# Kernel tuning notes

Hardware: AMD Instinct MI355X
Metric: run time of the kernel (lower is better)

The kernel has to match this reference:

```python
import jax, jax.numpy as jnp
import numpy as np


def setup_inputs() -> dict:
    key = jax.random.key(0)
    k1, k2, k3, k4 = jax.random.split(key, 4)
    B, S, E, H = 8, 2048, 1024, 64
    x = jax.random.normal(k1, (B, S, E), dtype=jnp.float32)
    scale = 1.0 / np.sqrt(E)
    Wq = jax.random.normal(k2, (E, H), dtype=jnp.float32) * scale
    Wk = jax.random.normal(k3, (E, H), dtype=jnp.float32) * scale
    Wv = jax.random.normal(k4, (E, H), dtype=jnp.float32) * scale
    return {"x": x, "Wq": Wq, "Wk": Wk, "Wv": Wv}


def reference(x, Wq, Wk, Wv):
    # x: [B, S, E]; Wq/Wk/Wv: [E, H]
    B, S, E = x.shape
    H = Wq.shape[1]
    q = x @ Wq  # [B, S, H]
    k = x @ Wk
    v = x @ Wv
    inv_sqrt_h = 1.0 / jnp.sqrt(jnp.asarray(H, dtype=x.dtype))
    att = jnp.einsum("bqh,bkh->bqk", q, k) * inv_sqrt_h  # [B, S, S]
    causal = jnp.tril(jnp.ones((S, S), dtype=bool))
    att = jnp.where(causal, att, jnp.asarray(-jnp.inf, dtype=att.dtype))
    att = jax.nn.softmax(att, axis=-1)
    # dropout p=0.0 (eval) -> identity
    return jnp.einsum("bqk,bkh->bqh", att, v)  # [B, S, H]
```

## Files before the change

kernel.cpp:

```cpp
#include <hip/hip_runtime.h>
#include <math.h>

typedef __attribute__((ext_vector_type(8))) short bf16x8;
typedef __attribute__((ext_vector_type(16))) float fx16;

#define SEQ 2048
#define HD 64

__device__ __forceinline__ unsigned f2bf_bits(float f){
  unsigned u = __float_as_uint(f);
  return (u + 0x7fffu + ((u >> 16) & 1u)) >> 16;
}
__device__ __forceinline__ unsigned cvt_pk_bf16(float a, float b){
  unsigned r;
  asm("v_cvt_pk_bf16_f32 %0, %1, %2" : "=v"(r) : "v"(a), "v"(b));
  return r;
}
__device__ __forceinline__ float lo16f(unsigned u){ return __uint_as_float(u << 16); }
__device__ __forceinline__ float hi16f(unsigned u){ return __uint_as_float(u & 0xffff0000u); }
union U8 { bf16x8 v; short s[8]; unsigned u[4]; };

__device__ __forceinline__ fx16 mfma_bf16(bf16x8 a, bf16x8 b, fx16 c){
  return __builtin_amdgcn_mfma_f32_32x32x16_bf16(a, b, c, 0, 0, 0);
}
__device__ __forceinline__ fx16 fzero(){
  fx16 z;
#pragma unroll
  for (int i = 0; i < 16; ++i) z[i] = 0.f;
  return z;
}

__global__ __launch_bounds__(256) void wconv_kernel(
    const float* __restrict__ Wq, const float* __restrict__ Wk, const float* __restrict__ Wv,
    short* __restrict__ wsB)
{
  int gid = blockIdx.x * 4 + (threadIdx.x >> 6);
  int lane = threadIdx.x & 63;
  int l31 = lane & 31, h = lane >> 5;
  int half = gid & 1;
  int rem = gid >> 1;
  int t = rem % 6;
  int stage = rem / 6;
  int n = t * 32 + l31;
  int mat = n >> 6, col = n & 63;
  const float* W = (mat == 0) ? Wq : (mat == 1) ? Wk : Wv;
  int kbase = stage * 16 + h * 8;
  U8 o;
#pragma unroll
  for (int i = 0; i < 8; ++i) {
    float f = W[(size_t)(kbase + i) * 64 + col];
    unsigned hb = f2bf_bits(f);
    if (half == 0) o.s[i] = (short)hb;
    else {
      float hf = __uint_as_float(hb << 16);
      o.s[i] = (short)f2bf_bits(f - hf);
    }
  }
  *(bf16x8*)(wsB + (size_t)gid * 512 + lane * 8) = o.v;
}

__global__ __launch_bounds__(256) void proj_kernel(
    const float* __restrict__ x, const short* __restrict__ wsB,
    short* __restrict__ qh, short* __restrict__ ql,
    short* __restrict__ kh, short* __restrict__ kl,
    short* __restrict__ vth, short* __restrict__ vtl)
{
  __shared__ float Rx[6 * 16 * 64];
  __shared__ float Vb[32 * 68];

  const int tid = threadIdx.x;
  const int lane = tid & 63, w = tid >> 6;
  const int l31 = lane & 31, h = lane >> 5;
  const int nsel = w & 1;
  const int ksel = w >> 1;
  const int row0 = blockIdx.x * 32;
  const size_t xbase = (size_t)(row0 + l31) * 1024;

  fx16 acc[3];
#pragma unroll
  for (int t = 0; t < 3; ++t) acc[t] = fzero();

#pragma unroll 4
  for (int s = 0; s < 32; ++s) {
    const int stage = ksel * 32 + s;
    const int k = stage * 16 + h * 8;
    float4 fa = *(const float4*)(x + xbase + k);
    float4 fb = *(const float4*)(x + xbase + k + 4);
    U8 ah, al;
    ah.u[0] = cvt_pk_bf16(fa.x, fa.y);
    ah.u[1] = cvt_pk_bf16(fa.z, fa.w);
    ah.u[2] = cvt_pk_bf16(fb.x, fb.y);
    ah.u[3] = cvt_pk_bf16(fb.z, fb.w);
    al.u[0] = cvt_pk_bf16(fa.x - lo16f(ah.u[0]), fa.y - hi16f(ah.u[0]));
    al.u[1] = cvt_pk_bf16(fa.z - lo16f(ah.u[1]), fa.w - hi16f(ah.u[1]));
    al.u[2] = cvt_pk_bf16(fb.x - lo16f(ah.u[2]), fb.y - hi16f(ah.u[2]));
    al.u[3] = cvt_pk_bf16(fb.z - lo16f(ah.u[3]), fb.w - hi16f(ah.u[3]));
#pragma unroll
    for (int tt = 0; tt < 3; ++tt) {
      const int tg = nsel * 3 + tt;
      const size_t g2 = ((size_t)stage * 6 + tg) * 2;
      bf16x8 Bh = *(const bf16x8*)(wsB + g2 * 512 + lane * 8);
      bf16x8 Bl = *(const bf16x8*)(wsB + g2 * 512 + 512 + lane * 8);
      acc[tt] = mfma_bf16(al.v, Bh, acc[tt]);
      acc[tt] = mfma_bf16(ah.v, Bl, acc[tt]);
      acc[tt] = mfma_bf16(ah.v, Bh, acc[tt]);
    }
  }

  if (ksel == 1) {
#pragma unroll
    for (int t = 0; t < 3; ++t) {
      const int tg = nsel * 3 + t;
#pragma unroll
      for (int r = 0; r < 16; ++r)
        Rx[tg * 1024 + r * 64 + lane] = acc[t][r];
    }
  }
  __syncthreads();
  if (ksel == 0) {
#pragma unroll
    for (int t = 0; t < 3; ++t) {
      const int tg = nsel * 3 + t;
      const int mat = tg >> 1;
      const int colb = (tg & 1) * 32 + l31;
      if (mat < 2) {
        short* dh = (mat == 0) ? qh : kh;
        short* dl = (mat == 0) ? ql : kl;
#pragma unroll
        for (int r = 0; r < 16; ++r) {
          float f = acc[t][r] + Rx[tg * 1024 + r * 64 + lane];
          int rowg = row0 + (r & 3) + 8 * (r >> 2) + 4 * h;
          unsigned hb = f2bf_bits(f);
          float hf = __uint_as_float(hb << 16);
          unsigned lb = f2bf_bits(f - hf);
          dh[(size_t)rowg * 64 + colb] = (short)hb;
          dl[(size_t)rowg * 64 + colb] = (short)lb;
        }
      } else {
#pragma unroll
        for (int r = 0; r < 16; ++r) {
          float f = acc[t][r] + Rx[tg * 1024 + r * 64 + lane];
          int srel = (r & 3) + 8 * (r >> 2) + 4 * h;
          Vb[srel * 68 + (tg - 4) * 32 + l31] = f;
        }
      }
    }
  }
  __syncthreads();
  {
    int d = tid >> 2, s8 = (tid & 3) * 8;
    int bb = row0 >> 11, s0 = row0 & 2047;
    U8 hv, lv;
#pragma unroll
    for (int ss = 0; ss < 8; ++ss) {
      float f = Vb[(s8 + ss) * 68 + d];
      unsigned hb = f2bf_bits(f);
      float hf = __uint_as_float(hb << 16);
      hv.s[ss] = (short)hb;
      lv.s[ss] = (short)f2bf_bits(f - hf);
    }
    size_t o = (size_t)(bb * 64 + d) * 2048 + s0 + s8;
    *(bf16x8*)(vth + o) = hv.v;
    *(bf16x8*)(vtl + o) = lv.v;
  }
}

__global__ __launch_bounds__(64) void attn_kernel(
    const short* __restrict__ qh, const short* __restrict__ ql,
    const short* __restrict__ kh, const short* __restrict__ kl,
    const short* __restrict__ vth, const short* __restrict__ vtl,
    float* __restrict__ segO, float* __restrict__ segL, float* __restrict__ segM)
{
  const int bid = blockIdx.x;
  const int b = bid & 7;
  const int r = bid >> 3;
  int g = 0;
  while (r >= 4 * (g + 1) * (g + 2)) ++g;
  const int rr = r - 4 * g * (g + 1);
  const int qt = g * 8 + rr / (g + 1);
  const int sg = rr % (g + 1);
  const int nk = qt + 1;
  const int nsg = g + 1;
  const int bs = nk / nsg, rem = nk % nsg;
  const int nsteps = bs + (sg < rem ? 1 : 0);
  const int kt0 = sg * bs + (sg < rem ? sg : rem);

  const int lane = threadIdx.x;
  const int l31 = lane & 31, h = lane >> 5;
  const int qabs = qt * 32 + l31;

  bf16x8 qf0[4], qf1[4];
  {
    size_t qrow = ((size_t)b * 2048 + qabs) * 64;
#pragma unroll
    for (int ds = 0; ds < 4; ++ds) {
      qf0[ds] = *(const bf16x8*)(qh + qrow + ds * 16 + 8 * h);
      qf1[ds] = *(const bf16x8*)(ql + qrow + ds * 16 + 8 * h);
    }
  }

  fx16 acc0 = fzero(), acc1 = fzero();
  float Mrun = -3e38f, lrun = 0.f;

  bf16x8 kah[4], kal[4];
  {
    const size_t koff = ((size_t)b * 2048 + (size_t)kt0 * 32 + l31) * 64 + 8 * h;
#pragma unroll
    for (int ds = 0; ds < 4; ++ds) {
      kah[ds] = *(const bf16x8*)(kh + koff + ds * 16);
      kal[ds] = *(const bf16x8*)(kl + koff + ds * 16);
    }
  }

  for (int it = 0; it < nsteps; ++it) {
    const int kt = kt0 + it;
    bf16x8 vfh[2][2], vfl[2][2];
#pragma unroll
    for (int kp = 0; kp < 2; ++kp)
#pragma unroll
      for (int md = 0; md < 2; ++md) {
        const size_t vrow = (size_t)(b * 64 + md * 32 + l31) * 2048 + kt * 32 + kp * 16 + 8 * h;
        vfh[kp][md] = *(const bf16x8*)(vth + vrow);
        vfl[kp][md] = *(const bf16x8*)(vtl + vrow);
      }
    const int kn = (it + 1 < nsteps) ? kt + 1 : kt;
    bf16x8 knh[4], knl[4];
    {
      const size_t koff = ((size_t)b * 2048 + (size_t)kn * 32 + l31) * 64 + 8 * h;
#pragma unroll
      for (int ds = 0; ds < 4; ++ds) {
        knh[ds] = *(const bf16x8*)(kh + koff + ds * 16);
        knl[ds] = *(const bf16x8*)(kl + koff + ds * 16);
      }
    }

    fx16 stA = fzero(), stB = fzero();
    __builtin_amdgcn_s_setprio(1);
#pragma unroll
    for (int ds = 0; ds < 4; ++ds) {
      stA = mfma_bf16(kah[ds], qf0[ds], stA);
      stB = mfma_bf16(kal[ds], qf0[ds], stB);
      stB = mfma_bf16(kah[ds], qf1[ds], stB);
    }
    __builtin_amdgcn_s_setprio(0);

    float sv[16];
    const bool diag = (kt == qt);
#pragma unroll
    for (int r2 = 0; r2 < 16; ++r2) {
      float s = (stA[r2] + stB[r2]) * 0.125f;
      if (diag) {
        int ka = kt * 32 + (r2 & 3) + 8 * (r2 >> 2) + 4 * h;
        if (ka > qabs) s = -3e38f;
      }
      sv[r2] = s;
    }
    float tm = sv[0];
#pragma unroll
    for (int r2 = 1; r2 < 16; ++r2) tm = fmaxf(tm, sv[r2]);
    tm = fmaxf(tm, __shfl_xor(tm, 32, 64));
    float Mnew = fmaxf(Mrun, tm);
    float alpha = __expf(Mrun - Mnew);
    Mrun = Mnew;
    float psum = 0.f;
#pragma unroll
    for (int r2 = 0; r2 < 16; ++r2) { sv[r2] = __expf(sv[r2] - Mnew); psum += sv[r2]; }
    psum += __shfl_xor(psum, 32, 64);
    lrun = lrun * alpha + psum;
#pragma unroll
    for (int r2 = 0; r2 < 16; ++r2) { acc0[r2] *= alpha; acc1[r2] *= alpha; }

    unsigned chv[8], clv[8];
#pragma unroll
    for (int q2 = 0; q2 < 8; ++q2) {
      unsigned c = cvt_pk_bf16(sv[2 * q2], sv[2 * q2 + 1]);
      chv[q2] = c;
      clv[q2] = cvt_pk_bf16(sv[2 * q2] - lo16f(c), sv[2 * q2 + 1] - hi16f(c));
    }
#pragma unroll
    for (int kp = 0; kp < 2; ++kp) {
      U8 ph, pl;
      {
        unsigned c0 = chv[4 * kp], c1 = chv[4 * kp + 1], c2 = chv[4 * kp + 2], c3 = chv[4 * kp + 3];
        unsigned x0 = (unsigned)__shfl_xor((int)c0, 32, 64);
        unsigned x1 = (unsigned)__shfl_xor((int)c1, 32, 64);
        unsigned x2 = (unsigned)__shfl_xor((int)c2, 32, 64);
        unsigned x3 = (unsigned)__shfl_xor((int)c3, 32, 64);
        ph.u[0] = h ? x2 : c0;  ph.u[1] = h ? x3 : c1;
        ph.u[2] = h ? c2 : x0;  ph.u[3] = h ? c3 : x1;
        c0 = clv[4 * kp]; c1 = clv[4 * kp + 1]; c2 = clv[4 * kp + 2]; c3 = clv[4 * kp + 3];
        x0 = (unsigned)__shfl_xor((int)c0, 32, 64);
        x1 = (unsigned)__shfl_xor((int)c1, 32, 64);
        x2 = (unsigned)__shfl_xor((int)c2, 32, 64);
        x3 = (unsigned)__shfl_xor((int)c3, 32, 64);
        pl.u[0] = h ? x2 : c0;  pl.u[1] = h ? x3 : c1;
        pl.u[2] = h ? c2 : x0;  pl.u[3] = h ? c3 : x1;
      }
      __builtin_amdgcn_s_setprio(1);
      acc0 = mfma_bf16(vfl[kp][0], ph.v, acc0);
      acc0 = mfma_bf16(vfh[kp][0], pl.v, acc0);
      acc0 = mfma_bf16(vfh[kp][0], ph.v, acc0);
      acc1 = mfma_bf16(vfl[kp][1], ph.v, acc1);
      acc1 = mfma_bf16(vfh[kp][1], pl.v, acc1);
      acc1 = mfma_bf16(vfh[kp][1], ph.v, acc1);
      __builtin_amdgcn_s_setprio(0);
    }
#pragma unroll
    for (int ds = 0; ds < 4; ++ds) { kah[ds] = knh[ds]; kal[ds] = knl[ds]; }
  }

  float* o = segO + (size_t)bid * 2048;
#pragma unroll
  for (int md = 0; md < 2; ++md) {
#pragma unroll
    for (int r2 = 0; r2 < 16; ++r2) {
      int d = md * 32 + (r2 & 3) + 8 * (r2 >> 2) + 4 * h;
      float val = md ? acc1[r2] : acc0[r2];
      o[d * 32 + l31] = val;
    }
  }
  if (h == 0) {
    segL[(size_t)bid * 32 + l31] = lrun;
    segM[(size_t)bid * 32 + l31] = Mrun;
  }
}

__global__ __launch_bounds__(256) void combine_kernel(
    const float* __restrict__ segO, const float* __restrict__ segL,
    const float* __restrict__ segM, float* __restrict__ out)
{
  __shared__ float Sc[8][32];
  __shared__ float Linv[32];
  __shared__ float Ot[64 * 40];

  const int bq = blockIdx.x;
  const int b = bq >> 6, qt = bq & 63;
  const int g = qt >> 3, nsg = g + 1;
  const int base = 4 * g * (g + 1) + (qt & 7) * nsg;
  const int tid = threadIdx.x;

  if (tid < 32) {
    float M = -3e38f;
    for (int s = 0; s < nsg; ++s)
      M = fmaxf(M, segM[(size_t)((base + s) * 8 + b) * 32 + tid]);
    float L = 0.f;
    for (int s = 0; s < nsg; ++s) {
      float e = __expf(segM[(size_t)((base + s) * 8 + b) * 32 + tid] - M);
      Sc[s][tid] = e;
      L += e * segL[(size_t)((base + s) * 8 + b) * 32 + tid];
    }
    Linv[tid] = 1.f / L;
  }
  __syncthreads();
  {
#pragma unroll
    for (int i = tid; i < 512; i += 256) {
      int d = i >> 3, q4 = (i & 7) * 4;
      float4 acc = {0.f, 0.f, 0.f, 0.f};
      for (int s = 0; s < nsg; ++s) {
        float4 v = *(const float4*)(segO + (size_t)((base + s) * 8 + b) * 2048 + d * 32 + q4);
        acc.x += Sc[s][q4 + 0] * v.x;
        acc.y += Sc[s][q4 + 1] * v.y;
        acc.z += Sc[s][q4 + 2] * v.z;
        acc.w += Sc[s][q4 + 3] * v.w;
      }
      *(float4*)&Ot[d * 40 + q4] = acc;
    }
  }
  __syncthreads();
  {
    const int q = tid >> 3, dc = (tid & 7) * 8;
    const float inv = Linv[q];
    float* dst = out + ((size_t)b * 2048 + qt * 32 + q) * 64 + dc;
#pragma unroll
    for (int i = 0; i < 2; ++i) {
      float4 o;
      o.x = Ot[(dc + 4 * i + 0) * 40 + q] * inv;
      o.y = Ot[(dc + 4 * i + 1) * 40 + q] * inv;
      o.z = Ot[(dc + 4 * i + 2) * 40 + q] * inv;
      o.w = Ot[(dc + 4 * i + 3) * 40 + q] * inv;
      *(float4*)(dst + 4 * i) = o;
    }
  }
}

extern "C" void kernel_launch(void* const* d_in, const int* in_sizes, int n_in,
                              void* d_out, int out_size, void* d_ws, size_t ws_size,
                              hipStream_t stream) {
  const float* x  = (const float*)d_in[0];
  const float* Wq = (const float*)d_in[1];
  const float* Wk = (const float*)d_in[2];
  const float* Wv = (const float*)d_in[3];

  char* wsb = (char*)d_ws;
  short* wsB = (short*)(wsb + 0);
  short* qh  = (short*)(wsb + 786432);
  short* ql  = (short*)(wsb + 2883584);
  short* kh  = (short*)(wsb + 4980736);
  short* kl  = (short*)(wsb + 7077888);
  short* vth = (short*)(wsb + 9175040);
  short* vtl = (short*)(wsb + 11272192);
  float* segO = (float*)(wsb + 13369344);
  float* segL = (float*)(wsb + 32243712);
  float* segM = (float*)(wsb + 32538624);

  wconv_kernel<<<192, 256, 0, stream>>>(Wq, Wk, Wv, wsB);
  proj_kernel<<<512, 256, 0, stream>>>(x, wsB, qh, ql, kh, kl, vth, vtl);
  attn_kernel<<<2304, 64, 0, stream>>>(qh, ql, kh, kl, vth, vtl, segO, segL, segM);
  combine_kernel<<<512, 256, 0, stream>>>(segO, segL, segM, (float*)d_out);
}
```

Measured before the change: 97.79 us.

## Stage projection operands in LDS and split attention into fixed five-tile segments

The projection kernel now runs six waves per block, one per output column tile, with the full K dimension in each wave. Weights go into LDS through async global_load_lds and x is converted to bf16 hi/lo in double-buffered LDS, which removes the split-K reduction through shared memory and the redundant global weight reads. The attention split changes to fixed segments of at most five key tiles, so there are more blocks (3536) with even work, and the K register prefetch is removed. The combine kernel adapts to the new segment indexing. In exchange there are more partial-segment writes and combine reads, and a barrier on every K chunk in the projection.

```diff
diff --git a/kernel.cpp b/kernel.cpp
--- a/kernel.cpp
+++ b/kernel.cpp
@@ -59,95 +59,106 @@
   *(bf16x8*)(wsB + (size_t)gid * 512 + lane * 8) = o.v;
 }
 
-__global__ __launch_bounds__(256) void proj_kernel(
+__global__ __launch_bounds__(384) void proj_kernel(
     const float* __restrict__ x, const short* __restrict__ wsB,
     short* __restrict__ qh, short* __restrict__ ql,
     short* __restrict__ kh, short* __restrict__ kl,
     short* __restrict__ vth, short* __restrict__ vtl)
 {
-  __shared__ float Rx[6 * 16 * 64];
+  __shared__ short Bs[2][12288];
+  __shared__ short Xs[2][2048];
   __shared__ float Vb[32 * 68];
 
   const int tid = threadIdx.x;
   const int lane = tid & 63, w = tid >> 6;
   const int l31 = lane & 31, h = lane >> 5;
-  const int nsel = w & 1;
-  const int ksel = w >> 1;
   const int row0 = blockIdx.x * 32;
-  const size_t xbase = (size_t)(row0 + l31) * 1024;
-
-  fx16 acc[3];
-#pragma unroll
-  for (int t = 0; t < 3; ++t) acc[t] = fzero();
-
-#pragma unroll 4
-  for (int s = 0; s < 32; ++s) {
-    const int stage = ksel * 32 + s;
-    const int k = stage * 16 + h * 8;
-    float4 fa = *(const float4*)(x + xbase + k);
-    float4 fb = *(const float4*)(x + xbase + k + 4);
-    U8 ah, al;
-    ah.u[0] = cvt_pk_bf16(fa.x, fa.y);
-    ah.u[1] = cvt_pk_bf16(fa.z, fa.w);
-    ah.u[2] = cvt_pk_bf16(fb.x, fb.y);
-    ah.u[3] = cvt_pk_bf16(fb.z, fb.w);
-    al.u[0] = cvt_pk_bf16(fa.x - lo16f(ah.u[0]), fa.y - hi16f(ah.u[0]));
-    al.u[1] = cvt_pk_bf16(fa.z - lo16f(ah.u[1]), fa.w - hi16f(ah.u[1]));
-    al.u[2] = cvt_pk_bf16(fb.x - lo16f(ah.u[2]), fb.y - hi16f(ah.u[2]));
-    al.u[3] = cvt_pk_bf16(fb.z - lo16f(ah.u[3]), fb.w - hi16f(ah.u[3]));
-#pragma unroll
-    for (int tt = 0; tt < 3; ++tt) {
-      const int tg = nsel * 3 + tt;
-      const size_t g2 = ((size_t)stage * 6 + tg) * 2;
-      bf16x8 Bh = *(const bf16x8*)(wsB + g2 * 512 + lane * 8);
-      bf16x8 Bl = *(const bf16x8*)(wsB + g2 * 512 + 512 + lane * 8);
-      acc[tt] = mfma_bf16(al.v, Bh, acc[tt]);
-      acc[tt] = mfma_bf16(ah.v, Bl, acc[tt]);
-      acc[tt] = mfma_bf16(ah.v, Bh, acc[tt]);
-    }
-  }
-
-  if (ksel == 1) {
-#pragma unroll
-    for (int t = 0; t < 3; ++t) {
-      const int tg = nsel * 3 + t;
-#pragma unroll
-      for (int r = 0; r < 16; ++r)
-        Rx[tg * 1024 + r * 64 + lane] = acc[t][r];
-    }
+
+  const int xrow = tid >> 3;
+  const int xk4 = tid & 7;
+  const int xs_slot = ((xk4 >> 2) * 2 + ((xk4 >> 1) & 1)) * 32 + xrow;
+  const int xs_e0 = (xk4 & 1) * 4;
+  const bool xthr = (tid < 256);
+
+  fx16 accP = fzero(), accQ = fzero();
+
+#define ISSUE_B(C)                                                        \
+  {                                                                       \
+    const char* bsrc = (const char*)wsB + (size_t)(C) * 24576;            \
+    char* bdst = (char*)&Bs[(C) & 1][0];                                  \
+    _Pragma("unroll")                                                     \
+    for (int i = 0; i < 4; ++i)                                           \
+      __builtin_amdgcn_global_load_lds(                                   \
+        (const __attribute__((address_space(1))) float*)(bsrc + i * 6144 + tid * 16), \
+        (__attribute__((address_space(3))) float*)(bdst + i * 6144 + tid * 16), 16, 0, 0); \
+  }
+
+#define WRITE_X(C, FX)                                                    \
+  {                                                                       \
+    unsigned h0 = cvt_pk_bf16(FX.x, FX.y), h1 = cvt_pk_bf16(FX.z, FX.w);  \
+    unsigned lz0 = cvt_pk_bf16(FX.x - lo16f(h0), FX.y - hi16f(h0));       \
+    unsigned lz1 = cvt_pk_bf16(FX.z - lo16f(h1), FX.w - hi16f(h1));       \
+    short* xb = &Xs[(C) & 1][0];                                          \
+    *(uint2*)&xb[xs_slot * 8 + xs_e0] = make_uint2(h0, h1);               \
+    *(uint2*)&xb[1024 + xs_slot * 8 + xs_e0] = make_uint2(lz0, lz1);      \
+  }
+
+  ISSUE_B(0);
+  if (xthr) {
+    float4 fx0 = *(const float4*)(x + (size_t)(row0 + xrow) * 1024 + xk4 * 4);
+    WRITE_X(0, fx0);
   }
   __syncthreads();
-  if (ksel == 0) {
-#pragma unroll
-    for (int t = 0; t < 3; ++t) {
-      const int tg = nsel * 3 + t;
-      const int mat = tg >> 1;
-      const int colb = (tg & 1) * 32 + l31;
-      if (mat < 2) {
-        short* dh = (mat == 0) ? qh : kh;
-        short* dl = (mat == 0) ? ql : kl;
-#pragma unroll
-        for (int r = 0; r < 16; ++r) {
-          float f = acc[t][r] + Rx[tg * 1024 + r * 64 + lane];
-          int rowg = row0 + (r & 3) + 8 * (r >> 2) + 4 * h;
-          unsigned hb = f2bf_bits(f);
-          float hf = __uint_as_float(hb << 16);
-          unsigned lb = f2bf_bits(f - hf);
-          dh[(size_t)rowg * 64 + colb] = (short)hb;
-          dl[(size_t)rowg * 64 + colb] = (short)lb;
-        }
-      } else {
-#pragma unroll
-        for (int r = 0; r < 16; ++r) {
-          float f = acc[t][r] + Rx[tg * 1024 + r * 64 + lane];
-          int srel = (r & 3) + 8 * (r >> 2) + 4 * h;
-          Vb[srel * 68 + (tg - 4) * 32 + l31] = f;
-        }
-      }
+
+  for (int c = 0; c < 32; ++c) {
+    const int buf = c & 1;
+    float4 fxn;
+    if (c < 31) {
+      ISSUE_B(c + 1);
+      if (xthr)
+        fxn = *(const float4*)(x + (size_t)(row0 + xrow) * 1024 + (c + 1) * 32 + xk4 * 4);
+    }
+#pragma unroll
+    for (int s = 0; s < 2; ++s) {
+      bf16x8 ah = *(const bf16x8*)&Xs[buf][((s * 2 + h) * 32 + l31) * 8];
+      bf16x8 al = *(const bf16x8*)&Xs[buf][1024 + ((s * 2 + h) * 32 + l31) * 8];
+      bf16x8 Bh = *(const bf16x8*)&Bs[buf][((s * 6 + w) * 2) * 512 + lane * 8];
+      bf16x8 Bl = *(const bf16x8*)&Bs[buf][((s * 6 + w) * 2 + 1) * 512 + lane * 8];
+      accP = mfma_bf16(ah, Bh, accP);
+      accQ = mfma_bf16(ah, Bl, accQ);
+      accQ = mfma_bf16(al, Bh, accQ);
+    }
+    if (c < 31 && xthr) WRITE_X(c + 1, fxn);
+    __syncthreads();
+  }
+#undef WRITE_X
+#undef ISSUE_B
+
+  if (w < 4) {
+    short* dh = (w < 2) ? qh : kh;
+    short* dl = (w < 2) ? ql : kl;
+    const int colb = (w & 1) * 32 + l31;
+#pragma unroll
+    for (int r = 0; r < 16; ++r) {
+      float f = accP[r] + accQ[r];
+      int rowg = row0 + (r & 3) + 8 * (r >> 2) + 4 * h;
+      unsigned hb = f2bf_bits(f);
+      float hf = __uint_as_float(hb << 16);
+      unsigned lb = f2bf_bits(f - hf);
+      dh[(size_t)rowg * 64 + colb] = (short)hb;
+      dl[(size_t)rowg * 64 + colb] = (short)lb;
+    }
+  } else {
+    const int colv = (w - 4) * 32 + l31;
+#pragma unroll
+    for (int r = 0; r < 16; ++r) {
+      float f = accP[r] + accQ[r];
+      int srel = (r & 3) + 8 * (r >> 2) + 4 * h;
+      Vb[srel * 68 + colv] = f;
     }
   }
   __syncthreads();
-  {
+  if (tid < 256) {
     int d = tid >> 2, s8 = (tid & 3) * 8;
     int bb = row0 >> 11, s0 = row0 & 2047;
     U8 hv, lv;
@@ -173,17 +184,13 @@
 {
   const int bid = blockIdx.x;
   const int b = bid & 7;
-  const int r = bid >> 3;
-  int g = 0;
-  while (r >= 4 * (g + 1) * (g + 2)) ++g;
-  const int rr = r - 4 * g * (g + 1);
-  const int qt = g * 8 + rr / (g + 1);
-  const int sg = rr % (g + 1);
+  int r = bid >> 3;
+  int qt = 0, acc = 0;
+  while (r >= acc + ((qt + 5) / 5)) { acc += (qt + 5) / 5; ++qt; }
+  const int sg = r - acc;
   const int nk = qt + 1;
-  const int nsg = g + 1;
-  const int bs = nk / nsg, rem = nk % nsg;
-  const int nsteps = bs + (sg < rem ? 1 : 0);
-  const int kt0 = sg * bs + (sg < rem ? sg : rem);
+  const int kt0 = sg * 5;
+  int nsteps = nk - kt0; if (nsteps > 5) nsteps = 5;
 
   const int lane = threadIdx.x;
   const int l31 = lane & 31, h = lane >> 5;
@@ -202,18 +209,17 @@
   fx16 acc0 = fzero(), acc1 = fzero();
   float Mrun = -3e38f, lrun = 0.f;
 
-  bf16x8 kah[4], kal[4];
-  {
-    const size_t koff = ((size_t)b * 2048 + (size_t)kt0 * 32 + l31) * 64 + 8 * h;
-#pragma unroll
-    for (int ds = 0; ds < 4; ++ds) {
-      kah[ds] = *(const bf16x8*)(kh + koff + ds * 16);
-      kal[ds] = *(const bf16x8*)(kl + koff + ds * 16);
-    }
-  }
-
   for (int it = 0; it < nsteps; ++it) {
     const int kt = kt0 + it;
+    bf16x8 kah[4], kal[4];
+    {
+      const size_t koff = ((size_t)b * 2048 + (size_t)kt * 32 + l31) * 64 + 8 * h;
+#pragma unroll
+      for (int ds = 0; ds < 4; ++ds) {
+        kah[ds] = *(const bf16x8*)(kh + koff + ds * 16);
+        kal[ds] = *(const bf16x8*)(kl + koff + ds * 16);
+      }
+    }
     bf16x8 vfh[2][2], vfl[2][2];
 #pragma unroll
     for (int kp = 0; kp < 2; ++kp)
@@ -223,16 +229,6 @@
         vfh[kp][md] = *(const bf16x8*)(vth + vrow);
         vfl[kp][md] = *(const bf16x8*)(vtl + vrow);
       }
-    const int kn = (it + 1 < nsteps) ? kt + 1 : kt;
-    bf16x8 knh[4], knl[4];
-    {
-      const size_t koff = ((size_t)b * 2048 + (size_t)kn * 32 + l31) * 64 + 8 * h;
-#pragma unroll
-      for (int ds = 0; ds < 4; ++ds) {
-        knh[ds] = *(const bf16x8*)(kh + koff + ds * 16);
-        knl[ds] = *(const bf16x8*)(kl + koff + ds * 16);
-      }
-    }
 
     fx16 stA = fzero(), stB = fzero();
     __builtin_amdgcn_s_setprio(1);
@@ -305,8 +301,6 @@
       acc1 = mfma_bf16(vfh[kp][1], ph.v, acc1);
       __builtin_amdgcn_s_setprio(0);
     }
-#pragma unroll
-    for (int ds = 0; ds < 4; ++ds) { kah[ds] = knh[ds]; kal[ds] = knl[ds]; }
   }
 
   float* o = segO + (size_t)bid * 2048;
@@ -329,14 +323,15 @@
     const float* __restrict__ segO, const float* __restrict__ segL,
     const float* __restrict__ segM, float* __restrict__ out)
 {
-  __shared__ float Sc[8][32];
+  __shared__ float Sc[13][32];
   __shared__ float Linv[32];
   __shared__ float Ot[64 * 40];
 
   const int bq = blockIdx.x;
   const int b = bq >> 6, qt = bq & 63;
-  const int g = qt >> 3, nsg = g + 1;
-  const int base = 4 * g * (g + 1) + (qt & 7) * nsg;
+  const int nsg = (qt + 5) / 5;
+  int base = 0;
+  for (int i = 0; i < qt; ++i) base += (i + 5) / 5;
   const int tid = threadIdx.x;
 
   if (tid < 32) {
@@ -356,15 +351,15 @@
 #pragma unroll
     for (int i = tid; i < 512; i += 256) {
       int d = i >> 3, q4 = (i & 7) * 4;
-      float4 acc = {0.f, 0.f, 0.f, 0.f};
+      float4 a = {0.f, 0.f, 0.f, 0.f};
       for (int s = 0; s < nsg; ++s) {
         float4 v = *(const float4*)(segO + (size_t)((base + s) * 8 + b) * 2048 + d * 32 + q4);
-        acc.x += Sc[s][q4 + 0] * v.x;
-        acc.y += Sc[s][q4 + 1] * v.y;
-        acc.z += Sc[s][q4 + 2] * v.z;
-        acc.w += Sc[s][q4 + 3] * v.w;
+        a.x += Sc[s][q4 + 0] * v.x;
+        a.y += Sc[s][q4 + 1] * v.y;
+        a.z += Sc[s][q4 + 2] * v.z;
+        a.w += Sc[s][q4 + 3] * v.w;
       }
-      *(float4*)&Ot[d * 40 + q4] = acc;
+      *(float4*)&Ot[d * 40 + q4] = a;
     }
   }
   __syncthreads();
@@ -401,11 +396,11 @@
   short* vth = (short*)(wsb + 9175040);
   short* vtl = (short*)(wsb + 11272192);
   float* segO = (float*)(wsb + 13369344);
-  float* segL = (float*)(wsb + 32243712);
-  float* segM = (float*)(wsb + 32538624);
+  float* segL = (float*)(wsb + 42336256);
+  float* segM = (float*)(wsb + 42788864);
 
   wconv_kernel<<<192, 256, 0, stream>>>(Wq, Wk, Wv, wsB);
-  proj_kernel<<<512, 256, 0, stream>>>(x, wsB, qh, ql, kh, kl, vth, vtl);
-  attn_kernel<<<2304, 64, 0, stream>>>(qh, ql, kh, kl, vth, vtl, segO, segL, segM);
+  proj_kernel<<<512, 384, 0, stream>>>(x, wsB, qh, ql, kh, kl, vth, vtl);
+  attn_kernel<<<3536, 64, 0, stream>>>(qh, ql, kh, kl, vth, vtl, segO, segL, segM);
   combine_kernel<<<512, 256, 0, stream>>>(segO, segL, segM, (float*)d_out);
 }
```

Result: slower. 120.7 us (+23.4%).
